# Optimization experiments

Measured on AMD Instinct MI355X. Metric: run time of the kernel, lower is better.

The kernel has to match this reference:

```python
import jax, jax.numpy as jnp
import numpy as np

N_DIMS = 1024
N_HEADS = 16
HEAD_DIM = N_DIMS // N_HEADS


def setup_inputs() -> dict:
    key = jax.random.key(0)
    k_x, k_wa, k_wp = jax.random.split(key, 3)
    x = jax.random.normal(k_x, (4, 2048, N_DIMS), dtype=jnp.float32)
    # nn.Linear weights stored [out, in]; apply as x @ W.T
    scale_a = 1.0 / np.sqrt(N_DIMS)
    w_attn = jax.random.uniform(k_wa, (3 * N_DIMS, N_DIMS), jnp.float32, -scale_a, scale_a)
    w_proj = jax.random.uniform(k_wp, (N_DIMS, N_DIMS), jnp.float32, -scale_a, scale_a)
    return {"x": x, "w_attn": w_attn, "w_proj": w_proj}


def reference(x, w_attn, w_proj):
    B, S, D = x.shape
    qkv = x @ w_attn.T                                  # [B, S, 3D]
    q, k, v = jnp.split(qkv, 3, axis=-1)
    # [B, H, S, Dh]
    def heads(t):
        return t.reshape(B, S, N_HEADS, HEAD_DIM).transpose(0, 2, 1, 3)
    q, k, v = heads(q), heads(k), heads(v)
    scores = jnp.einsum('bhqd,bhkd->bhqk', q, k) * (1.0 / np.sqrt(HEAD_DIM))
    causal = jnp.tril(jnp.ones((S, S), dtype=bool))
    scores = jnp.where(causal[None, None], scores, -jnp.inf)
    attn = jax.nn.softmax(scores, axis=-1)              # dropout: eval mode (identity)
    y = jnp.einsum('bhqk,bhkd->bhqd', attn, v)
    y = y.transpose(0, 2, 1, 3).reshape(B, S, D)
    return y @ w_proj.T
```

## Files before the change

### kernel.cpp

```cpp
#include <hip/hip_runtime.h>

typedef unsigned short ushort_t;
typedef __attribute__((ext_vector_type(8))) short bf16x8;
typedef __attribute__((ext_vector_type(4))) float f32x4;


__device__ __forceinline__ ushort_t f2bf(float f) {
    union { float f; unsigned u; } c; c.f = f;
    unsigned u = c.u;
    unsigned r = (u + 0x7fffu + ((u >> 16) & 1u)) >> 16;
    return (ushort_t)r;
}

__device__ __forceinline__ unsigned pk_bf16(float a, float b) {
    unsigned r;
    asm("v_cvt_pk_bf16_f32 %0, %1, %2" : "=v"(r) : "v"(a), "v"(b));
    return r;
}

__device__ __forceinline__ void gld_lds16(const ushort_t* g, ushort_t* l) {
    __builtin_amdgcn_global_load_lds(
        (const __attribute__((address_space(1))) void*)g,
        (__attribute__((address_space(3))) void*)l, 16, 0, 0);
}


__global__ void convert_bf16(const float* __restrict__ in, ushort_t* __restrict__ out, int n4) {
    int i = blockIdx.x * blockDim.x + threadIdx.x;
    if (i < n4) {
        const float4 f = ((const float4*)in)[i];
        ushort4 o;
        o.x = f2bf(f.x); o.y = f2bf(f.y); o.z = f2bf(f.z); o.w = f2bf(f.w);
        ((ushort4*)out)[i] = o;
    }
}


__global__ __launch_bounds__(256) void gemm_qkv(
    const ushort_t* __restrict__ A, const ushort_t* __restrict__ W,
    ushort_t* __restrict__ qo, ushort_t* __restrict__ ko, ushort_t* __restrict__ vto)
{
    constexpr int K = 1024;
    const int m0 = blockIdx.x * 128;
    const int n0 = blockIdx.y * 128;
    __shared__ alignas(16) ushort_t smem[16384];
    ushort_t* sA = smem;
    ushort_t* sB = smem + 8192;
    const int tid = threadIdx.x;
    const int wave = tid >> 6, lane = tid & 63;
    const int quad = lane >> 4, l16 = lane & 15;
    const int l8 = lane & 7;
    const int wm = (wave >> 1) << 6, wn = (wave & 1) << 6;
    const int srow8 = lane >> 3;
    const int sg = ((l8 ^ srow8) << 3);

    f32x4 acc[4][4] = {};
    const ushort_t* aRow0 = A + (size_t)(m0 + wave * 32 + srow8) * K + sg;
    const ushort_t* bRow0 = W + (size_t)(n0 + wave * 32 + srow8) * K + sg;

    for (int k0 = 0; k0 < K; k0 += 64) {
#pragma unroll
        for (int c = 0; c < 4; ++c) {
            gld_lds16(aRow0 + (size_t)c * 8 * K + k0, sA + (wave * 4 + c) * 512);
            gld_lds16(bRow0 + (size_t)c * 8 * K + k0, sB + (wave * 4 + c) * 512);
        }
        __syncthreads();
#pragma unroll
        for (int ks = 0; ks < 2; ++ks) {
            bf16x8 af[4], bfr[4];
#pragma unroll
            for (int f = 0; f < 4; ++f) {
                const int rg = (((ks * 4 + quad) ^ l8) << 3);
                af[f]  = *(const bf16x8*)(sA + (wm + f * 16 + l16) * 64 + rg);
                bfr[f] = *(const bf16x8*)(sB + (wn + f * 16 + l16) * 64 + rg);
            }
#pragma unroll
            for (int mf = 0; mf < 4; ++mf)
#pragma unroll
                for (int nf = 0; nf < 4; ++nf)
                    acc[mf][nf] = __builtin_amdgcn_mfma_f32_16x16x32_bf16(af[mf], bfr[nf], acc[mf][nf], 0, 0, 0);
        }
        __syncthreads();
    }

    const int which = n0 >> 10;
    ushort_t* sT = smem + wave * 2048;
    const int b  = (m0 + wm) >> 11;
    const int sb = (m0 + wm) & 2047;
    const int h  = ((n0 + wn) & 1023) >> 6;
    const int bh = b * 16 + h;

    if (which < 2) {
        ushort_t* go = (which == 0) ? qo : ko;
        const float qs1 = (which == 0) ? 0.18033688011112042f : 1.0f;
#pragma unroll
        for (int mf = 0; mf < 4; ++mf) {
#pragma unroll
            for (int nf = 0; nf < 4; ++nf)
#pragma unroll
                for (int i = 0; i < 4; ++i) {
                    const int mll = quad * 4 + i;
                    sT[mll * 64 + ((nf * 16 + l16) ^ (4 * (mll & 7)))] = f2bf(acc[mf][nf][i] * qs1);
                }
            __builtin_amdgcn_s_waitcnt(0);
#pragma unroll
            for (int p = 0; p < 4; ++p) {
                const int mll = p * 4 + quad;
                const ushort4 val = *(const ushort4*)(sT + mll * 64 + ((l16 * 4) ^ (4 * (mll & 7))));
                const int s = sb + mf * 16 + mll;
                *(ushort4*)(go + ((size_t)bh * 2048 + s) * 64 + l16 * 4) = val;
            }
            __builtin_amdgcn_s_waitcnt(0);
        }
    } else {
#pragma unroll
        for (int nf = 0; nf < 4; ++nf) {
#pragma unroll
            for (int mf = 0; mf < 4; ++mf) {
                ushort4 w;
                w.x = f2bf(acc[mf][nf][0]);
                w.y = f2bf(acc[mf][nf][1]);
                w.z = f2bf(acc[mf][nf][2]);
                w.w = f2bf(acc[mf][nf][3]);
                *(ushort4*)(sT + l16 * 64 + ((mf * 16 + quad * 4) ^ (4 * (l16 & 7)))) = w;
            }
            __builtin_amdgcn_s_waitcnt(0);
#pragma unroll
            for (int p = 0; p < 4; ++p) {
                const int nll = p * 4 + quad;
                const ushort4 val = *(const ushort4*)(sT + nll * 64 + ((l16 * 4) ^ (4 * (nll & 7))));
                const int dh = nf * 16 + nll;
                *(ushort4*)(vto + ((size_t)bh * 64 + dh) * 2048 + sb + l16 * 4) = val;
            }
            __builtin_amdgcn_s_waitcnt(0);
        }
    }
}


__global__ __launch_bounds__(256) void attn(
    const ushort_t* __restrict__ qg_, const ushort_t* __restrict__ kg_,
    const ushort_t* __restrict__ vg_, ushort_t* __restrict__ y)
{
    const int bh = blockIdx.x;
    const int b = bh >> 4, h = bh & 15;
    const int tid = threadIdx.x, wave = tid >> 6, lane = tid & 63;
    const int quad = lane >> 4, l16 = lane & 15;
    const int l8 = lane & 7;

    __shared__ alignas(16) ushort_t sQP[4096];
    __shared__ alignas(16) ushort_t sK[4096];
    __shared__ alignas(16) ushort_t sV[4096];

    const ushort_t* kg = kg_ + (size_t)bh * 2048 * 64;
    const ushort_t* vg = vg_ + (size_t)bh * 64 * 2048;

    const int srow8 = lane >> 3;
    const int sg = ((l8 ^ srow8) << 3);
    ushort_t* sPw = sQP + wave * 1024;

    const int qy = 31 - (int)blockIdx.y;
    const int q0 = qy * 64;

    {
        const ushort_t* qg = qg_ + ((size_t)bh * 2048 + q0 + wave * 16) * 64;
#pragma unroll
        for (int c = 0; c < 2; ++c)
            gld_lds16(qg + (size_t)(c * 8 + srow8) * 64 + sg, sQP + (wave * 2 + c) * 512);
    }
    __builtin_amdgcn_s_waitcnt(0);

    bf16x8 bq[2];
#pragma unroll
    for (int ks = 0; ks < 2; ++ks)
        bq[ks] = *(const bf16x8*)(sQP + (wave * 16 + l16) * 64 + (((ks * 4 + quad) ^ l8) << 3));

    f32x4 oacc[4] = {};
    f32x4 lpv = {0.f, 0.f, 0.f, 0.f};

    const int wrow = q0 + wave * 16 + l16;

    for (int t = 0; t <= qy; ++t) {
        const int k0 = t * 64;
        __syncthreads();
#pragma unroll
        for (int c = 0; c < 2; ++c) {
            const int chunk = wave * 2 + c;
            gld_lds16(kg + (size_t)(k0 + chunk * 8 + srow8) * 64 + sg, sK + chunk * 512);
            gld_lds16(vg + (size_t)(chunk * 8 + srow8) * 2048 + k0 + sg, sV + chunk * 512);
        }
        __syncthreads();

        f32x4 sacc[4] = {};
#pragma unroll
        for (int ks = 0; ks < 2; ++ks) {
            bf16x8 ak[4];
#pragma unroll
            for (int kf = 0; kf < 4; ++kf)
                ak[kf] = *(const bf16x8*)(sK + (kf * 16 + l16) * 64 + (((ks * 4 + quad) ^ l8) << 3));
#pragma unroll
            for (int kf = 0; kf < 4; ++kf)
                sacc[kf] = __builtin_amdgcn_mfma_f32_16x16x32_bf16(ak[kf], bq[ks], sacc[kf], 0, 0, 0);
        }

        const bool diag = (t == qy);
#pragma unroll
        for (int kf = 0; kf < 4; ++kf) {
            float pv[4];
#pragma unroll
            for (int i = 0; i < 4; ++i) {
                float sv = sacc[kf][i];
                if (diag) {
                    const int cg = k0 + kf * 16 + quad * 4 + i;
                    sv = (cg <= wrow) ? sv : -3.0e38f;
                }
                pv[i] = __builtin_amdgcn_exp2f(sv);
                lpv[i] += pv[i];
            }
            const unsigned w0 = pk_bf16(pv[0], pv[1]);
            const unsigned w1 = pk_bf16(pv[2], pv[3]);
            const int c0 = kf * 16 + quad * 4;
            *(uint2*)(sPw + l16 * 64 + (((c0 >> 3) ^ l8) << 3) + (c0 & 7)) =
                make_uint2(w0, w1);
        }
        asm volatile("" ::: "memory");

#pragma unroll
        for (int ks = 0; ks < 2; ++ks) {
            const int rgrp = (((ks * 4 + quad) ^ l8) << 3);
            const bf16x8 pa = *(const bf16x8*)(sPw + l16 * 64 + rgrp);
            bf16x8 vb[4];
#pragma unroll
            for (int nf = 0; nf < 4; ++nf)
                vb[nf] = *(const bf16x8*)(sV + (nf * 16 + l16) * 64 + rgrp);
#pragma unroll
            for (int nf = 0; nf < 4; ++nf)
                oacc[nf] = __builtin_amdgcn_mfma_f32_16x16x32_bf16(pa, vb[nf], oacc[nf], 0, 0, 0);
        }
    }

    float rs = (lpv[0] + lpv[1]) + (lpv[2] + lpv[3]);
    rs += __shfl_xor(rs, 16);
    rs += __shfl_xor(rs, 32);
#pragma unroll
    for (int i = 0; i < 4; ++i) {
        const float inv = 1.0f / __shfl(rs, quad * 4 + i);
        const int r = q0 + wave * 16 + quad * 4 + i;
#pragma unroll
        for (int nf = 0; nf < 4; ++nf)
            y[((size_t)b * 2048 + r) * 1024 + h * 64 + nf * 16 + l16] =
                f2bf(oacc[nf][i] * inv);
    }
}


__global__ __launch_bounds__(256) void gemm_proj(
    const ushort_t* __restrict__ A, const ushort_t* __restrict__ W, float* __restrict__ out)
{
    constexpr int K = 1024;
    const int m0 = blockIdx.x * 128;
    const int n0 = blockIdx.y * 128;
    __shared__ alignas(16) ushort_t smem[16384];
    ushort_t* sA = smem;
    ushort_t* sB = smem + 8192;
    const int tid = threadIdx.x;
    const int wave = tid >> 6, lane = tid & 63;
    const int quad = lane >> 4, l16 = lane & 15;
    const int l8 = lane & 7;
    const int wm = (wave >> 1) << 6, wn = (wave & 1) << 6;
    const int srow8 = lane >> 3;
    const int sg = ((l8 ^ srow8) << 3);

    f32x4 acc[4][4] = {};
    const ushort_t* aRow0 = A + (size_t)(m0 + wave * 32 + srow8) * K + sg;
    const ushort_t* bRow0 = W + (size_t)(n0 + wave * 32 + srow8) * K + sg;

    for (int k0 = 0; k0 < K; k0 += 64) {
#pragma unroll
        for (int c = 0; c < 4; ++c) {
            gld_lds16(aRow0 + (size_t)c * 8 * K + k0, sA + (wave * 4 + c) * 512);
            gld_lds16(bRow0 + (size_t)c * 8 * K + k0, sB + (wave * 4 + c) * 512);
        }
        __syncthreads();
#pragma unroll
        for (int ks = 0; ks < 2; ++ks) {
            bf16x8 af[4], bfr[4];
#pragma unroll
            for (int f = 0; f < 4; ++f) {
                const int rg = (((ks * 4 + quad) ^ l8) << 3);
                af[f]  = *(const bf16x8*)(sA + (wm + f * 16 + l16) * 64 + rg);
                bfr[f] = *(const bf16x8*)(sB + (wn + f * 16 + l16) * 64 + rg);
            }
#pragma unroll
            for (int mf = 0; mf < 4; ++mf)
#pragma unroll
                for (int nf = 0; nf < 4; ++nf)
                    acc[mf][nf] = __builtin_amdgcn_mfma_f32_16x16x32_bf16(af[mf], bfr[nf], acc[mf][nf], 0, 0, 0);
        }
        __syncthreads();
    }

#pragma unroll
    for (int mf = 0; mf < 4; ++mf)
#pragma unroll
        for (int nf = 0; nf < 4; ++nf)
#pragma unroll
            for (int i = 0; i < 4; ++i) {
                const int m = m0 + wm + mf * 16 + quad * 4 + i;
                const int n = n0 + wn + nf * 16 + l16;
                out[(size_t)m * 1024 + n] = acc[mf][nf][i];
            }
}


extern "C" void kernel_launch(void* const* d_in, const int* in_sizes, int n_in,
                              void* d_out, int out_size, void* d_ws, size_t ws_size,
                              hipStream_t stream) {
    const float* x  = (const float*)d_in[0];
    const float* wa = (const float*)d_in[1];
    const float* wp = (const float*)d_in[2];
    float* out = (float*)d_out;

    char* ws = (char*)d_ws;
    ushort_t* xb  = (ushort_t*)(ws);
    ushort_t* wab = (ushort_t*)(ws + 16777216);
    ushort_t* wpb = (ushort_t*)(ws + 16777216 + 6291456);
    ushort_t* q   = (ushort_t*)(ws + 25165824);
    ushort_t* k   = (ushort_t*)(ws + 41943040);
    ushort_t* vt  = (ushort_t*)(ws + 58720256);
    ushort_t* y   = xb;

    convert_bf16<<<8192 * 1024 / 4 / 256, 256, 0, stream>>>(x, xb, 8192 * 1024 / 4);
    convert_bf16<<<3072 * 1024 / 4 / 256, 256, 0, stream>>>(wa, wab, 3072 * 1024 / 4);
    convert_bf16<<<1024 * 1024 / 4 / 256, 256, 0, stream>>>(wp, wpb, 1024 * 1024 / 4);

    gemm_qkv<<<dim3(64, 24), 256, 0, stream>>>(xb, wab, q, k, vt);
    attn<<<dim3(64, 32), 256, 0, stream>>>(q, k, vt, y);
    gemm_proj<<<dim3(64, 8), 256, 0, stream>>>(y, wpb, out);
}
```

Baseline: 235.0 us.

## Double query tile per attention block to reuse K/V tiles across 32 rows per wave

Each attention block now covers 128 query rows instead of 64, so every wave handles two 16-row query fragments. The K and V tiles staged in LDS are shared by twice as many rows, which halves global K/V traffic and the number of blocks. Q is loaded straight from global memory into registers instead of through LDS. Causal skipping is done per wave and per fragment. This raises register and LDS use, gives fewer blocks (1024) to spread over the CUs, and leaves waves idle at barriers on tiles they skip.

```diff
diff --git a/kernel.cpp b/kernel.cpp
--- a/kernel.cpp
+++ b/kernel.cpp
@@ -148,7 +148,7 @@
     const int quad = lane >> 4, l16 = lane & 15;
     const int l8 = lane & 7;
 
-    __shared__ alignas(16) ushort_t sQP[4096];
+    __shared__ alignas(16) ushort_t sP[8192];
     __shared__ alignas(16) ushort_t sK[4096];
     __shared__ alignas(16) ushort_t sV[4096];
 
@@ -157,30 +157,27 @@
 
     const int srow8 = lane >> 3;
     const int sg = ((l8 ^ srow8) << 3);
-    ushort_t* sPw = sQP + wave * 1024;
-
-    const int qy = 31 - (int)blockIdx.y;
-    const int q0 = qy * 64;
-
-    {
-        const ushort_t* qg = qg_ + ((size_t)bh * 2048 + q0 + wave * 16) * 64;
-#pragma unroll
-        for (int c = 0; c < 2; ++c)
-            gld_lds16(qg + (size_t)(c * 8 + srow8) * 64 + sg, sQP + (wave * 2 + c) * 512);
-    }
-    __builtin_amdgcn_s_waitcnt(0);
-
-    bf16x8 bq[2];
-#pragma unroll
-    for (int ks = 0; ks < 2; ++ks)
-        bq[ks] = *(const bf16x8*)(sQP + (wave * 16 + l16) * 64 + (((ks * 4 + quad) ^ l8) << 3));
-
-    f32x4 oacc[4] = {};
-    f32x4 lpv = {0.f, 0.f, 0.f, 0.f};
-
-    const int wrow = q0 + wave * 16 + l16;
-
-    for (int t = 0; t <= qy; ++t) {
+
+    const int qt = 15 - (int)blockIdx.y;
+    const int q0 = qt * 128;
+    const int wbase = q0 + wave * 32;
+
+    bf16x8 bq[2][2];
+#pragma unroll
+    for (int qh = 0; qh < 2; ++qh)
+#pragma unroll
+        for (int ks = 0; ks < 2; ++ks)
+            bq[qh][ks] = *(const bf16x8*)(qg_ +
+                ((size_t)bh * 2048 + wbase + qh * 16 + l16) * 64 + ks * 32 + quad * 8);
+
+    f32x4 oacc[2][4] = {};
+    f32x4 lpv[2] = {};
+
+    ushort_t* sP0 = sP + (wave * 2 + 0) * 1024;
+    ushort_t* sP1 = sP + (wave * 2 + 1) * 1024;
+
+    const int tmax = 2 * qt + 1;
+    for (int t = 0; t <= tmax; ++t) {
         const int k0 = t * 64;
         __syncthreads();
 #pragma unroll
@@ -191,65 +188,83 @@
         }
         __syncthreads();
 
-        f32x4 sacc[4] = {};
-#pragma unroll
-        for (int ks = 0; ks < 2; ++ks) {
-            bf16x8 ak[4];
-#pragma unroll
-            for (int kf = 0; kf < 4; ++kf)
-                ak[kf] = *(const bf16x8*)(sK + (kf * 16 + l16) * 64 + (((ks * 4 + quad) ^ l8) << 3));
-#pragma unroll
-            for (int kf = 0; kf < 4; ++kf)
-                sacc[kf] = __builtin_amdgcn_mfma_f32_16x16x32_bf16(ak[kf], bq[ks], sacc[kf], 0, 0, 0);
-        }
-
-        const bool diag = (t == qy);
+        const bool act0 = (k0 <= wbase + 15);
+        const bool act1 = (k0 <= wbase + 31);
+        if (!act1) continue;
+
 #pragma unroll
         for (int kf = 0; kf < 4; ++kf) {
-            float pv[4];
-#pragma unroll
-            for (int i = 0; i < 4; ++i) {
-                float sv = sacc[kf][i];
-                if (diag) {
-                    const int cg = k0 + kf * 16 + quad * 4 + i;
-                    sv = (cg <= wrow) ? sv : -3.0e38f;
+            const bf16x8 ak0 = *(const bf16x8*)(sK + (kf * 16 + l16) * 64 + ((quad ^ l8) << 3));
+            const bf16x8 ak1 = *(const bf16x8*)(sK + (kf * 16 + l16) * 64 + (((4 + quad) ^ l8) << 3));
+            f32x4 s0 = {}, s1 = {};
+            if (act0) {
+                s0 = __builtin_amdgcn_mfma_f32_16x16x32_bf16(ak0, bq[0][0], s0, 0, 0, 0);
+                s0 = __builtin_amdgcn_mfma_f32_16x16x32_bf16(ak1, bq[0][1], s0, 0, 0, 0);
+            }
+            s1 = __builtin_amdgcn_mfma_f32_16x16x32_bf16(ak0, bq[1][0], s1, 0, 0, 0);
+            s1 = __builtin_amdgcn_mfma_f32_16x16x32_bf16(ak1, bq[1][1], s1, 0, 0, 0);
+
+#pragma unroll
+            for (int qh = 0; qh < 2; ++qh) {
+                if (qh == 0 && !act0) continue;
+                const f32x4 sv = (qh == 0) ? s0 : s1;
+                const bool msk = (k0 + 63 > wbase + qh * 16);
+                const int wrow = wbase + qh * 16 + l16;
+                float pv[4];
+#pragma unroll
+                for (int i = 0; i < 4; ++i) {
+                    float x = sv[i];
+                    if (msk) {
+                        const int cg = k0 + kf * 16 + quad * 4 + i;
+                        x = (cg <= wrow) ? x : -3.0e38f;
+                    }
+                    pv[i] = __builtin_amdgcn_exp2f(x);
                 }
-                pv[i] = __builtin_amdgcn_exp2f(sv);
-                lpv[i] += pv[i];
-            }
-            const unsigned w0 = pk_bf16(pv[0], pv[1]);
-            const unsigned w1 = pk_bf16(pv[2], pv[3]);
-            const int c0 = kf * 16 + quad * 4;
-            *(uint2*)(sPw + l16 * 64 + (((c0 >> 3) ^ l8) << 3) + (c0 & 7)) =
-                make_uint2(w0, w1);
+                lpv[qh][0] += pv[0]; lpv[qh][1] += pv[1];
+                lpv[qh][2] += pv[2]; lpv[qh][3] += pv[3];
+                const unsigned w0 = pk_bf16(pv[0], pv[1]);
+                const unsigned w1 = pk_bf16(pv[2], pv[3]);
+                const int c0 = kf * 16 + quad * 4;
+                *(uint2*)(((qh == 0) ? sP0 : sP1) + l16 * 64 +
+                          (((c0 >> 3) ^ l8) << 3) + (c0 & 7)) = make_uint2(w0, w1);
+            }
         }
         asm volatile("" ::: "memory");
 
 #pragma unroll
         for (int ks = 0; ks < 2; ++ks) {
             const int rgrp = (((ks * 4 + quad) ^ l8) << 3);
-            const bf16x8 pa = *(const bf16x8*)(sPw + l16 * 64 + rgrp);
             bf16x8 vb[4];
 #pragma unroll
             for (int nf = 0; nf < 4; ++nf)
                 vb[nf] = *(const bf16x8*)(sV + (nf * 16 + l16) * 64 + rgrp);
+            const bf16x8 pa1 = *(const bf16x8*)(sP1 + l16 * 64 + rgrp);
 #pragma unroll
             for (int nf = 0; nf < 4; ++nf)
-                oacc[nf] = __builtin_amdgcn_mfma_f32_16x16x32_bf16(pa, vb[nf], oacc[nf], 0, 0, 0);
-        }
-    }
-
-    float rs = (lpv[0] + lpv[1]) + (lpv[2] + lpv[3]);
-    rs += __shfl_xor(rs, 16);
-    rs += __shfl_xor(rs, 32);
-#pragma unroll
-    for (int i = 0; i < 4; ++i) {
-        const float inv = 1.0f / __shfl(rs, quad * 4 + i);
-        const int r = q0 + wave * 16 + quad * 4 + i;
-#pragma unroll
-        for (int nf = 0; nf < 4; ++nf)
-            y[((size_t)b * 2048 + r) * 1024 + h * 64 + nf * 16 + l16] =
-                f2bf(oacc[nf][i] * inv);
+                oacc[1][nf] = __builtin_amdgcn_mfma_f32_16x16x32_bf16(pa1, vb[nf], oacc[1][nf], 0, 0, 0);
+            if (act0) {
+                const bf16x8 pa0 = *(const bf16x8*)(sP0 + l16 * 64 + rgrp);
+#pragma unroll
+                for (int nf = 0; nf < 4; ++nf)
+                    oacc[0][nf] = __builtin_amdgcn_mfma_f32_16x16x32_bf16(pa0, vb[nf], oacc[0][nf], 0, 0, 0);
+            }
+        }
+    }
+
+#pragma unroll
+    for (int qh = 0; qh < 2; ++qh) {
+        float rs = (lpv[qh][0] + lpv[qh][1]) + (lpv[qh][2] + lpv[qh][3]);
+        rs += __shfl_xor(rs, 16);
+        rs += __shfl_xor(rs, 32);
+#pragma unroll
+        for (int i = 0; i < 4; ++i) {
+            const float inv = 1.0f / __shfl(rs, quad * 4 + i);
+            const int r = wbase + qh * 16 + quad * 4 + i;
+#pragma unroll
+            for (int nf = 0; nf < 4; ++nf)
+                y[((size_t)b * 2048 + r) * 1024 + h * 64 + nf * 16 + l16] =
+                    f2bf(oacc[qh][nf][i] * inv);
+        }
     }
 }
 
@@ -335,6 +350,6 @@
     convert_bf16<<<1024 * 1024 / 4 / 256, 256, 0, stream>>>(wp, wpb, 1024 * 1024 / 4);
 
     gemm_qkv<<<dim3(64, 24), 256, 0, stream>>>(xb, wab, q, k, vt);
-    attn<<<dim3(64, 32), 256, 0, stream>>>(q, k, vt, y);
+    attn<<<dim3(64, 16), 256, 0, stream>>>(q, k, vt, y);
     gemm_proj<<<dim3(64, 8), 256, 0, stream>>>(y, wpb, out);
 }
```

Measured after the change: 240.0 us. +2.1%, slower.

## Fuse bf16 conversions into one launch and pass P via permlane swaps

Applied to the files above, without the earlier changes.

The three fp32-to-bf16 conversion launches are merged into one kernel that picks its source buffer by global index, removing two launch overheads. In the attention kernel, the softmax probabilities no longer round-trip through LDS to change from the MFMA output layout to the A-operand layout. They are packed to bf16 in registers and rearranged across lanes with v_permlane32_swap/v_permlane16_swap. This removes LDS writes and reads and a barrier-like dependency per tile, but relies on the swap pattern matching the key ordering the V fragments expect.

```diff
diff --git a/kernel.cpp b/kernel.cpp
--- a/kernel.cpp
+++ b/kernel.cpp
@@ -25,14 +25,19 @@
 }
 
 
-__global__ void convert_bf16(const float* __restrict__ in, ushort_t* __restrict__ out, int n4) {
-    int i = blockIdx.x * blockDim.x + threadIdx.x;
-    if (i < n4) {
-        const float4 f = ((const float4*)in)[i];
-        ushort4 o;
-        o.x = f2bf(f.x); o.y = f2bf(f.y); o.z = f2bf(f.z); o.w = f2bf(f.w);
-        ((ushort4*)out)[i] = o;
-    }
+__global__ __launch_bounds__(256) void convert_all(
+    const float* __restrict__ x, const float* __restrict__ wa, const float* __restrict__ wp,
+    ushort_t* __restrict__ xb, ushort_t* __restrict__ wab, ushort_t* __restrict__ wpb)
+{
+    const int i = blockIdx.x * blockDim.x + threadIdx.x;
+    const float* src; ushort_t* dst; int j;
+    if (i < 2097152)      { src = x;  dst = xb;  j = i; }
+    else if (i < 2883584) { src = wa; dst = wab; j = i - 2097152; }
+    else                  { src = wp; dst = wpb; j = i - 2883584; }
+    const float4 f = ((const float4*)src)[j];
+    ushort4 o;
+    o.x = f2bf(f.x); o.y = f2bf(f.y); o.z = f2bf(f.z); o.w = f2bf(f.w);
+    ((ushort4*)dst)[j] = o;
 }
 
 
@@ -148,7 +153,7 @@
     const int quad = lane >> 4, l16 = lane & 15;
     const int l8 = lane & 7;
 
-    __shared__ alignas(16) ushort_t sQP[4096];
+    __shared__ alignas(16) ushort_t sQ[4096];
     __shared__ alignas(16) ushort_t sK[4096];
     __shared__ alignas(16) ushort_t sV[4096];
 
@@ -157,7 +162,6 @@
 
     const int srow8 = lane >> 3;
     const int sg = ((l8 ^ srow8) << 3);
-    ushort_t* sPw = sQP + wave * 1024;
 
     const int qy = 31 - (int)blockIdx.y;
     const int q0 = qy * 64;
@@ -166,14 +170,14 @@
         const ushort_t* qg = qg_ + ((size_t)bh * 2048 + q0 + wave * 16) * 64;
 #pragma unroll
         for (int c = 0; c < 2; ++c)
-            gld_lds16(qg + (size_t)(c * 8 + srow8) * 64 + sg, sQP + (wave * 2 + c) * 512);
+            gld_lds16(qg + (size_t)(c * 8 + srow8) * 64 + sg, sQ + (wave * 2 + c) * 512);
     }
     __builtin_amdgcn_s_waitcnt(0);
 
     bf16x8 bq[2];
 #pragma unroll
     for (int ks = 0; ks < 2; ++ks)
-        bq[ks] = *(const bf16x8*)(sQP + (wave * 16 + l16) * 64 + (((ks * 4 + quad) ^ l8) << 3));
+        bq[ks] = *(const bf16x8*)(sQ + (wave * 16 + l16) * 64 + (((ks * 4 + quad) ^ l8) << 3));
 
     f32x4 oacc[4] = {};
     f32x4 lpv = {0.f, 0.f, 0.f, 0.f};
@@ -204,6 +208,7 @@
         }
 
         const bool diag = (t == qy);
+        unsigned Xp0[4], Xp1[4];
 #pragma unroll
         for (int kf = 0; kf < 4; ++kf) {
             float pv[4];
@@ -217,25 +222,34 @@
                 pv[i] = __builtin_amdgcn_exp2f(sv);
                 lpv[i] += pv[i];
             }
-            const unsigned w0 = pk_bf16(pv[0], pv[1]);
-            const unsigned w1 = pk_bf16(pv[2], pv[3]);
-            const int c0 = kf * 16 + quad * 4;
-            *(uint2*)(sPw + l16 * 64 + (((c0 >> 3) ^ l8) << 3) + (c0 & 7)) =
-                make_uint2(w0, w1);
-        }
-        asm volatile("" ::: "memory");
+            Xp0[kf] = pk_bf16(pv[0], pv[1]);
+            Xp1[kf] = pk_bf16(pv[2], pv[3]);
+        }
+
+        bf16x8 pa[2];
+#pragma unroll
+        for (int ks = 0; ks < 2; ++ks) {
+            unsigned a0 = Xp0[2 * ks], b0 = Xp0[2 * ks + 1];
+            asm("v_permlane32_swap_b32 %0, %1" : "+v"(a0), "+v"(b0));
+            asm("v_permlane16_swap_b32 %0, %1" : "+v"(a0), "+v"(b0));
+            unsigned a1 = Xp1[2 * ks], b1 = Xp1[2 * ks + 1];
+            asm("v_permlane32_swap_b32 %0, %1" : "+v"(a1), "+v"(b1));
+            asm("v_permlane16_swap_b32 %0, %1" : "+v"(a1), "+v"(b1));
+            union { unsigned u4[4]; bf16x8 v; } P;
+            P.u4[0] = a0; P.u4[1] = a1; P.u4[2] = b0; P.u4[3] = b1;
+            pa[ks] = P.v;
+        }
 
 #pragma unroll
         for (int ks = 0; ks < 2; ++ks) {
             const int rgrp = (((ks * 4 + quad) ^ l8) << 3);
-            const bf16x8 pa = *(const bf16x8*)(sPw + l16 * 64 + rgrp);
             bf16x8 vb[4];
 #pragma unroll
             for (int nf = 0; nf < 4; ++nf)
                 vb[nf] = *(const bf16x8*)(sV + (nf * 16 + l16) * 64 + rgrp);
 #pragma unroll
             for (int nf = 0; nf < 4; ++nf)
-                oacc[nf] = __builtin_amdgcn_mfma_f32_16x16x32_bf16(pa, vb[nf], oacc[nf], 0, 0, 0);
+                oacc[nf] = __builtin_amdgcn_mfma_f32_16x16x32_bf16(pa[ks], vb[nf], oacc[nf], 0, 0, 0);
         }
     }
 
@@ -330,9 +344,7 @@
     ushort_t* vt  = (ushort_t*)(ws + 58720256);
     ushort_t* y   = xb;
 
-    convert_bf16<<<8192 * 1024 / 4 / 256, 256, 0, stream>>>(x, xb, 8192 * 1024 / 4);
-    convert_bf16<<<3072 * 1024 / 4 / 256, 256, 0, stream>>>(wa, wab, 3072 * 1024 / 4);
-    convert_bf16<<<1024 * 1024 / 4 / 256, 256, 0, stream>>>(wp, wpb, 1024 * 1024 / 4);
+    convert_all<<<12288, 256, 0, stream>>>(x, wa, wp, xb, wab, wpb);
 
     gemm_qkv<<<dim3(64, 24), 256, 0, stream>>>(xb, wab, q, k, vt);
     attn<<<dim3(64, 32), 256, 0, stream>>>(q, k, vt, y);
```

Measured after the change: 225.9 us. 3.9% less time.
